# Optimization experiments

Measured on AMD Instinct MI355X. Metric: run time of the kernel, lower is better.

The kernel has to match this reference:

```python
import jax, jax.numpy as jnp
import numpy as np

B, L, D = 4, 2048, 512
NL, ED, N, R, K = 2, 1024, 16, 32, 4
EPS = 1e-5


def rmsnorm(x, w):
    return x * jax.lax.rsqrt(jnp.mean(x * x, axis=-1, keepdims=True) + EPS) * w


def mamba_block(u, in_w, conv_w, conv_b, xproj_w, dtproj_w, dtproj_b, A_log, Dp, out_w):
    # u: [B, L, D]
    xz = u @ in_w.T                              # [B, L, 2*ED]
    xp, z = jnp.split(xz, 2, axis=-1)
    # depthwise causal conv1d over time
    xc = jnp.transpose(xp, (0, 2, 1))            # [B, ED, L]
    w = conv_w[:, None, :]                       # [ED, 1, K]
    xc = jax.lax.conv_general_dilated(
        xc, w, window_strides=(1,), padding=[(K - 1, 0)],
        feature_group_count=ED, dimension_numbers=('NCH', 'OIH', 'NCH'))
    xc = jnp.transpose(xc, (0, 2, 1)) + conv_b   # [B, L, ED]
    xc = jax.nn.silu(xc)
    # input-dependent SSM params
    dbc = xc @ xproj_w.T                         # [B, L, R+2N]
    dt, Bm, Cm = jnp.split(dbc, [R, R + N], axis=-1)
    delta = jax.nn.softplus(dt @ dtproj_w.T + dtproj_b)  # [B, L, ED]
    A = -jnp.exp(A_log)                          # [ED, N]
    # sequential selective scan over time (carry h: [B, ED, N])
    dT = jnp.transpose(delta, (1, 0, 2))
    BT = jnp.transpose(Bm, (1, 0, 2))
    CT = jnp.transpose(Cm, (1, 0, 2))
    xT = jnp.transpose(xc, (1, 0, 2))

    def step(h, inp):
        d_t, B_t, C_t, x_t = inp                 # [B,ED], [B,N], [B,N], [B,ED]
        dA = jnp.exp(d_t[..., None] * A)         # [B, ED, N]
        h = dA * h + (d_t * x_t)[..., None] * B_t[:, None, :]
        y = jnp.einsum('ben,bn->be', h, C_t)
        return h, y

    h0 = jnp.zeros((u.shape[0], ED, N), u.dtype)
    _, yT = jax.lax.scan(step, h0, (dT, BT, CT, xT))
    y = jnp.transpose(yT, (1, 0, 2)) + Dp * xc   # [B, L, ED]
    y = y * jax.nn.silu(z)
    return y @ out_w.T                           # [B, L, D]


def setup_inputs() -> dict:
    key = jax.random.key(0)
    ks = jax.random.split(key, 10)
    s = 0.02
    return {
        'x': jax.random.normal(ks[0], (B, L, D), jnp.float32),
        'mask': jnp.ones((B, L), jnp.int32),
        'norm_w': jnp.ones((NL, D), jnp.float32),
        'in_w': jax.random.normal(ks[1], (NL, 2 * ED, D), jnp.float32) * s,
        'conv_w': jax.random.normal(ks[2], (NL, ED, K), jnp.float32) * 0.2,
        'conv_b': jnp.zeros((NL, ED), jnp.float32),
        'xproj_w': jax.random.normal(ks[3], (NL, R + 2 * N, ED), jnp.float32) * s,
        'dtproj_w': jax.random.normal(ks[4], (NL, ED, R), jnp.float32) * s,
        'dtproj_b': jax.random.normal(ks[5], (NL, ED), jnp.float32) * 0.1,
        'A_log': jnp.broadcast_to(jnp.log(jnp.arange(1, N + 1, dtype=jnp.float32)), (NL, ED, N)) + 0.0,
        'D_param': jnp.ones((NL, ED), jnp.float32),
        'out_w': jax.random.normal(ks[6], (NL, D, ED), jnp.float32) * s,
    }


def reference(x, mask, norm_w, in_w, conv_w, conv_b, xproj_w, dtproj_w,
              dtproj_b, A_log, D_param, out_w):
    m = mask.astype(x.dtype)[:, :, None]
    for i in range(norm_w.shape[0]):
        x = x * m
        # ResidualBlock: x + MambaBlock(RMSNorm(x)); dropout is identity at eval
        x = x + mamba_block(rmsnorm(x, norm_w[i]), in_w[i], conv_w[i], conv_b[i],
                            xproj_w[i], dtproj_w[i], dtproj_b[i], A_log[i],
                            D_param[i], out_w[i])
        x = x * m
    return x, x[:, 0, :]
```

## Files before the change

### kernel.cpp

```cpp
#include <hip/hip_runtime.h>
#include <math.h>

#define B_ 4
#define L_ 2048
#define D_ 512
#define ED_ 1024
#define N_ 16
#define R_ 32
#define KC_ 4
#define M_ (B_*L_)
#define NC_ 128
#define T_  (L_/NC_)
#define S_  (B_*ED_*N_)
#define BE_ (B_*ED_)
#define LOG2E 1.44269504f
#define LN2   0.69314718f

typedef __attribute__((ext_vector_type(8))) short short8;
typedef __attribute__((ext_vector_type(4))) float floatx4;
typedef __attribute__((ext_vector_type(2))) float floatv2;

static __device__ __forceinline__ float b2f(unsigned short u) {
    unsigned int v = ((unsigned int)u) << 16;
    float f;
    __builtin_memcpy(&f, &v, 4);
    return f;
}
static __device__ __forceinline__ unsigned short f2b(float f) {
    unsigned int u;
    __builtin_memcpy(&u, &f, 4);
    unsigned int lsb = (u >> 16) & 1u;
    u += 0x7fffu + lsb;
    return (unsigned short)(u >> 16);
}
static __device__ __forceinline__ float silu(float x) {
    return x / (1.f + exp2f(-LOG2E * x));
}
static __device__ __forceinline__ float softplusf(float x) {
    return fmaxf(x, 0.f) + LN2 * log2f(1.f + exp2f(-LOG2E * fabsf(x)));
}
static __device__ __forceinline__ void pow_tree2(float a1, floatv2* pw) {
    float a2 = a1 * a1, a4 = a2 * a2, a8 = a4 * a4;
    pw[0] = (floatv2){a1, a2};
    pw[1] = pw[0] * a2;
    pw[2] = pw[0] * a4;
    pw[3] = pw[1] * a4;
    pw[4] = pw[0] * a8;
    pw[5] = pw[1] * a8;
    pw[6] = pw[2] * a8;
    pw[7] = pw[3] * a8;
}

__global__ void k_flag0(int* flag) {
    if (blockIdx.x == 0 && threadIdx.x == 0) *flag = 0;
}
__global__ void k_detect(const unsigned short* __restrict__ x, int* flag) {
    int i = blockIdx.x * 256 + threadIdx.x;
    unsigned int e = (x[i] >> 7) & 0xFF;
    unsigned long long m = __ballot(e >= 0x88);
    if ((threadIdx.x & 63) == 0 && m != 0ull) atomicOr(flag, 1);
}

struct Seg9 { const void* src[9]; int prefix[10]; };
__global__ void k_cvt_batch(Seg9 segs, float* __restrict__ dst, int total,
                            const int* __restrict__ flag) {
    int i = blockIdx.x * 256 + threadIdx.x;
    if (i >= total) return;
    int s = 0;
#pragma unroll
    for (int k = 1; k < 9; ++k) if (i >= segs.prefix[k]) s = k;
    int off = i - segs.prefix[s];
    if (*flag) dst[i] = ((const float*)segs.src[s])[off];
    else       dst[i] = b2f(((const unsigned short*)segs.src[s])[off]);
}
__global__ void k_cvt_bf_batch(const void* __restrict__ src0,
                               const void* __restrict__ src1,
                               unsigned short* __restrict__ dst,
                               int n0, int total, const int* __restrict__ flag) {
    int i = blockIdx.x * 256 + threadIdx.x;
    if (i >= total) return;
    const void* src = (i < n0) ? src0 : src1;
    int off = (i < n0) ? i : i - n0;
    if (*flag) dst[i] = f2b(((const float*)src)[off]);
    else       dst[i] = ((const unsigned short*)src)[off];
}

__global__ void k_prep(const float* __restrict__ wdt,
                       const float* __restrict__ A_log,
                       float* __restrict__ wT,
                       float* __restrict__ A0s,
                       int* __restrict__ structf) {
    int idx = blockIdx.x * 256 + threadIdx.x;
    int layer = idx >> 10, e = idx & (ED_ - 1);
    const float* src = wdt + (size_t)idx * R_;
    float* dstb = wT + (size_t)layer * (R_ * ED_);
#pragma unroll
    for (int r = 0; r < R_; ++r)
        dstb[(r >> 2) * (ED_ * 4) + e * 4 + (r & 3)] = src[r];
    float A0 = -exp2f(LOG2E * A_log[(size_t)idx * N_]) * LOG2E;
    bool st = true;
#pragma unroll
    for (int n = 1; n < N_; ++n) {
        float An = -exp2f(LOG2E * A_log[(size_t)idx * N_ + n]) * LOG2E;
        st = st && (fabsf(An - (n + 1) * A0) <= 1e-4f * fabsf(An));
    }
    A0s[idx] = A0;
    structf[idx] = st ? 1 : 0;
}

__global__ __launch_bounds__(128) void k_rmsnorm(float* __restrict__ x,
                                                 const int* __restrict__ mask,
                                                 const float* __restrict__ w,
                                                 unsigned short* __restrict__ ubf) {
    int row = blockIdx.x;
    int tid = threadIdx.x;
    size_t base = (size_t)row * D_ + tid * 4;
    float4 v = *(const float4*)(x + base);
    float mv = (float)mask[row];
    v.x *= mv; v.y *= mv; v.z *= mv; v.w *= mv;
    *(float4*)(x + base) = v;
    float ss = v.x*v.x + v.y*v.y + v.z*v.z + v.w*v.w;
#pragma unroll
    for (int o = 1; o < 64; o <<= 1) ss += __shfl_xor(ss, o, 64);
    __shared__ float sred[2];
    if ((tid & 63) == 0) sred[tid >> 6] = ss;
    __syncthreads();
    float rs = rsqrtf((sred[0] + sred[1]) / (float)D_ + 1e-5f);
    float4 wv = *(const float4*)(w + tid * 4);
    ushort4 b4;
    b4.x = f2b(v.x * rs * wv.x);
    b4.y = f2b(v.y * rs * wv.y);
    b4.z = f2b(v.z * rs * wv.z);
    b4.w = f2b(v.w * rs * wv.w);
    *(ushort4*)(ubf + base) = b4;
}

typedef __attribute__((address_space(1))) const unsigned int guint;
typedef __attribute__((address_space(3))) unsigned int luint;
#define GLL(gp, lp) __builtin_amdgcn_global_load_lds((guint*)(const void*)(gp), (luint*)(void*)(lp), 16, 0, 0)

template<int N> static __device__ __forceinline__ void waitv() {
    if constexpr (N == 0) asm volatile("s_waitcnt vmcnt(0)" ::: "memory");
    else if constexpr (N == 3) asm volatile("s_waitcnt vmcnt(3)" ::: "memory");
    else if constexpr (N == 4) asm volatile("s_waitcnt vmcnt(4)" ::: "memory");
}

template<int MODE, int BNT>
__global__ __launch_bounds__(256) void gemm_bt(const unsigned short* __restrict__ A,
                                               const unsigned short* __restrict__ W,
                                               void* __restrict__ C,
                                               const int* __restrict__ mask,
                                               const int* __restrict__ flag,
                                               void* __restrict__ out,
                                               int M, int N, int K) {
    constexpr int NF = BNT / 32;
    constexpr int LW = 2 + BNT / 64;
    __shared__ unsigned short As[3][128][32];
    __shared__ unsigned short Bs[3][BNT][32];
    int tid  = threadIdx.x;
    int wave = tid >> 6;
    int lane = tid & 63;
    int nwg = gridDim.x * gridDim.y;
    int id  = blockIdx.y * gridDim.x + blockIdx.x;
    int swz = (id & 7) * (nwg >> 3) + (id >> 3);
    int m0 = (swz / gridDim.x) * 128;
    int n0 = (swz % gridDim.x) * BNT;
    int wm = (wave & 1) * 64;
    int wn = (wave >> 1) * (BNT / 2);
    int quad = lane >> 4;
    int l16  = lane & 15;
    int crd = (quad ^ ((l16 >> 1) & 3)) * 8;

    int rA0 = wave * 16 + (lane >> 2);
    int cA  = ((lane & 3) ^ ((rA0 >> 1) & 3)) * 8;

    floatx4 acc[4][NF] = {};

    auto stage = [&](int buf, int k0) {
        const unsigned short* gA0 = A + (size_t)(m0 + rA0) * K + k0 + cA;
        GLL(gA0,                   &As[buf][wave * 16][0]);
        GLL(gA0 + (size_t)64 * K,  &As[buf][64 + wave * 16][0]);
        const unsigned short* gB0 = W + (size_t)(n0 + rA0) * K + k0 + cA;
        GLL(gB0,                   &Bs[buf][wave * 16][0]);
        if constexpr (BNT == 128)
            GLL(gB0 + (size_t)64 * K, &Bs[buf][64 + wave * 16][0]);
    };

    int nk = K / 32;
    stage(0, 0);
    stage(1, 32);

    int cur = 0;
    for (int t = 0; t < nk; ++t) {
        if (t + 1 < nk) waitv<LW>();
        else            waitv<0>();
        asm volatile("s_barrier" ::: "memory");
        if (t + 2 < nk) {
            int bw = cur + 2; if (bw >= 3) bw -= 3;
            stage(bw, (t + 2) * 32);
        }
        short8 af[4], bfr[NF];
#pragma unroll
        for (int f = 0; f < 4; ++f)
            af[f]  = *(const short8*)&As[cur][wm + f * 16 + l16][crd];
#pragma unroll
        for (int f = 0; f < NF; ++f)
            bfr[f] = *(const short8*)&Bs[cur][wn + f * 16 + l16][crd];
#pragma unroll
        for (int mf = 0; mf < 4; ++mf)
#pragma unroll
            for (int nf = 0; nf < NF; ++nf)
                acc[mf][nf] = __builtin_amdgcn_mfma_f32_16x16x32_bf16(af[mf], bfr[nf], acc[mf][nf], 0, 0, 0);
        asm volatile("s_waitcnt lgkmcnt(0)" ::: "memory");
        cur = (cur == 2) ? 0 : cur + 1;
    }

    int fl = (MODE == 3) ? *flag : 0;
#pragma unroll
    for (int mf = 0; mf < 4; ++mf) {
#pragma unroll
        for (int nf = 0; nf < NF; ++nf) {
#pragma unroll
            for (int i = 0; i < 4; ++i) {
                int r = m0 + wm + mf * 16 + quad * 4 + i;
                int c = n0 + wn + nf * 16 + l16;
                size_t idx = (size_t)r * N + c;
                if (MODE == 1) {
                    ((unsigned short*)C)[idx] = f2b(acc[mf][nf][i]);
                } else if (MODE == 2) {
                    float* C32 = (float*)C;
                    float mv = (float)mask[r];
                    C32[idx] = (C32[idx] + acc[mf][nf][i]) * mv;
                } else {
                    const float* C32 = (const float*)C;
                    float mv = (float)mask[r];
                    float v = (C32[idx] + acc[mf][nf][i]) * mv;
                    if (fl) ((float*)out)[idx] = v;
                    else    ((unsigned short*)out)[idx] = f2b(v);
                    if ((r & (L_ - 1)) == 0) {
                        size_t oidx = (size_t)M_ * D_ + (size_t)(r >> 11) * D_ + c;
                        if (fl) ((float*)out)[oidx] = v;
                        else    ((unsigned short*)out)[oidx] = f2b(v);
                    }
                }
            }
        }
    }
}

#define BM 64
#define BN 64
#define BK 16
#define KS 8
__global__ __launch_bounds__(256) void gemm_nt_sk(const unsigned short* __restrict__ A,
                                                  const float* __restrict__ W,
                                                  float* __restrict__ part,
                                                  int M, int N, int K) {
    __shared__ float Asm[BK][BM + 4];
    __shared__ float Wsm[BK][BN + 4];
    int tid = threadIdx.x;
    int ks = blockIdx.x;
    int m0 = blockIdx.y * BM;
    int kb = ks * (K / KS);
    int ke = kb + (K / KS);
    int tx = tid & 15;
    int ty = tid >> 4;
    int lr = tid >> 2;
    int lk = (tid & 3) * 4;
    float acc[4][4] = {};
    for (int k0 = kb; k0 < ke; k0 += BK) {
        ushort4 av = *(const ushort4*)(A + (size_t)(m0 + lr) * K + k0 + lk);
        Asm[lk + 0][lr] = b2f(av.x); Asm[lk + 1][lr] = b2f(av.y);
        Asm[lk + 2][lr] = b2f(av.z); Asm[lk + 3][lr] = b2f(av.w);
        float4 wv = *(const float4*)(W + (size_t)lr * K + k0 + lk);
        Wsm[lk + 0][lr] = wv.x; Wsm[lk + 1][lr] = wv.y;
        Wsm[lk + 2][lr] = wv.z; Wsm[lk + 3][lr] = wv.w;
        __syncthreads();
#pragma unroll
        for (int kk = 0; kk < BK; ++kk) {
            float4 a = *(const float4*)&Asm[kk][ty * 4];
            float4 w = *(const float4*)&Wsm[kk][tx * 4];
            acc[0][0] += a.x * w.x; acc[0][1] += a.x * w.y; acc[0][2] += a.x * w.z; acc[0][3] += a.x * w.w;
            acc[1][0] += a.y * w.x; acc[1][1] += a.y * w.y; acc[1][2] += a.y * w.z; acc[1][3] += a.y * w.w;
            acc[2][0] += a.z * w.x; acc[2][1] += a.z * w.y; acc[2][2] += a.z * w.z; acc[2][3] += a.z * w.w;
            acc[3][0] += a.w * w.x; acc[3][1] += a.w * w.y; acc[3][2] += a.w * w.z; acc[3][3] += a.w * w.w;
        }
        __syncthreads();
    }
    float* p = part + (size_t)ks * M * N;
#pragma unroll
    for (int i = 0; i < 4; ++i) {
        int m = m0 + ty * 4 + i;
#pragma unroll
        for (int j = 0; j < 4; ++j) {
            int n = tx * 4 + j;
            p[(size_t)m * N + n] = acc[i][j];
        }
    }
}

__global__ void k_red8(const float* __restrict__ part, float* __restrict__ dbc, int mn4) {
    int i = blockIdx.x * 256 + threadIdx.x;
    if (i >= mn4) return;
    float4 s = ((const float4*)part)[i];
#pragma unroll
    for (int ks = 1; ks < KS; ++ks) {
        float4 v = ((const float4*)(part + (size_t)ks * mn4 * 4))[i];
        s.x += v.x; s.y += v.y; s.z += v.z; s.w += v.w;
    }
    ((float4*)dbc)[i] = s;
}

__global__ __launch_bounds__(256) void k_conv(const unsigned short* __restrict__ xzb,
                                              const float* __restrict__ cw,
                                              const float* __restrict__ cb,
                                              unsigned short* __restrict__ xcb) {
    int idx = blockIdx.x * 256 + threadIdx.x;
    int e2 = idx & (ED_ / 2 - 1);
    int e  = e2 * 2;
    int bl = idx >> 9;
    int l  = bl & (L_ - 1);
    float acc0 = cb[e], acc1 = cb[e + 1];
    const unsigned short* col = xzb + (size_t)bl * (2 * ED_) + e;
    float4 wa = *(const float4*)(cw + e * 4);
    float4 wb = *(const float4*)(cw + e * 4 + 4);
    ushort2 v3 = *(const ushort2*)(col);
    if (l >= 3) {
        ushort2 v0 = *(const ushort2*)(col - 3 * 2 * ED_);
        ushort2 v1 = *(const ushort2*)(col - 2 * 2 * ED_);
        ushort2 v2 = *(const ushort2*)(col - 1 * 2 * ED_);
        acc0 += wa.x * b2f(v0.x) + wa.y * b2f(v1.x) + wa.z * b2f(v2.x) + wa.w * b2f(v3.x);
        acc1 += wb.x * b2f(v0.y) + wb.y * b2f(v1.y) + wb.z * b2f(v2.y) + wb.w * b2f(v3.y);
    } else {
        if (l >= 2) {
            ushort2 v1 = *(const ushort2*)(col - 2 * 2 * ED_);
            acc0 += wa.y * b2f(v1.x); acc1 += wb.y * b2f(v1.y);
        }
        if (l >= 1) {
            ushort2 v2 = *(const ushort2*)(col - 1 * 2 * ED_);
            acc0 += wa.z * b2f(v2.x); acc1 += wb.z * b2f(v2.y);
        }
        acc0 += wa.w * b2f(v3.x); acc1 += wb.w * b2f(v3.y);
    }
    ushort2 o;
    o.x = f2b(silu(acc0));
    o.y = f2b(silu(acc1));
    *(ushort2*)(xcb + (size_t)bl * ED_ + e) = o;
}

__global__ __launch_bounds__(256) void k_scan_a(const unsigned short* __restrict__ xcb,
                                                const float* __restrict__ dbc,
                                                const float* __restrict__ wt,
                                                const float* __restrict__ dtb,
                                                const float* __restrict__ A0s,
                                                const int* __restrict__ structf,
                                                const float* __restrict__ A_log,
                                                float* __restrict__ sumdbuf,
                                                float* __restrict__ hl) {
    int b = blockIdx.z, c = blockIdx.y;
    int e = blockIdx.x * 256 + threadIdx.x;
    __shared__ float sRow[T_][64];
    size_t t0 = (size_t)b * L_ + (size_t)c * T_;
    {
        const float4* src = (const float4*)(dbc + t0 * 64);
        float4* dst = (float4*)&sRow[0][0];
#pragma unroll
        for (int i = 0; i < T_ * 16; i += 256)
            dst[i + threadIdx.x] = src[i + threadIdx.x];
    }
    __syncthreads();
    floatv2 w2[R_ / 2];
    {
        const float4* wtp = (const float4*)wt;
#pragma unroll
        for (int i = 0; i < 8; ++i) {
            float4 v = wtp[(size_t)i * ED_ + e];
            w2[2 * i]     = (floatv2){v.x, v.y};
            w2[2 * i + 1] = (floatv2){v.z, v.w};
        }
    }
    float bias = dtb[e];
    float A0 = A0s[e];
    bool structured = structf[e] != 0;
    floatv2 h2[8];
#pragma unroll
    for (int i = 0; i < 8; ++i) h2[i] = (floatv2){0.f, 0.f};
    float sumd = 0.f;
    if (structured) {
        const unsigned short* xp = xcb + t0 * ED_ + e;
        float xv_t = b2f(*xp); xp += ED_;
        for (int t = 0; t < T_; ++t) {
            unsigned short xr = (t + 1 < T_) ? *xp : (unsigned short)0; xp += ED_;
            const floatv2* dt2 = (const floatv2*)&sRow[t][0];
            floatv2 q0 = {0.f, 0.f}, q1 = {0.f, 0.f}, q2 = {0.f, 0.f}, q3 = {0.f, 0.f};
#pragma unroll
            for (int r = 0; r < R_ / 2; r += 4) {
                q0 += dt2[r + 0] * w2[r + 0];
                q1 += dt2[r + 1] * w2[r + 1];
                q2 += dt2[r + 2] * w2[r + 2];
                q3 += dt2[r + 3] * w2[r + 3];
            }
            floatv2 qs = (q0 + q1) + (q2 + q3);
            float d = softplusf(qs.x + qs.y + bias);
            float dx = d * xv_t;
            sumd += d;
            floatv2 pw[8];
            pow_tree2(exp2f(d * A0), pw);
            const floatv2* bb2 = (const floatv2*)&sRow[t][32];
#pragma unroll
            for (int i = 0; i < 8; ++i)
                h2[i] = pw[i] * h2[i] + dx * bb2[i];
            xv_t = b2f(xr);
        }
    } else {
        float A[N_];
        float* h = (float*)h2;
#pragma unroll
        for (int n = 0; n < N_; ++n) A[n] = -exp2f(LOG2E * A_log[e * N_ + n]) * LOG2E;
        float* wsc = (float*)w2;
        for (int t = 0; t < T_; ++t) {
            size_t bl = t0 + t;
            float p0 = bias, p1 = 0.f, p2 = 0.f, p3 = 0.f;
#pragma unroll
            for (int r = 0; r < R_; r += 4) {
                p0 += sRow[t][r + 0] * wsc[r + 0];
                p1 += sRow[t][r + 1] * wsc[r + 1];
                p2 += sRow[t][r + 2] * wsc[r + 2];
                p3 += sRow[t][r + 3] * wsc[r + 3];
            }
            float d = softplusf((p0 + p1) + (p2 + p3));
            float dx = d * b2f(xcb[bl * ED_ + e]);
            sumd += d;
#pragma unroll
            for (int n = 0; n < N_; ++n) {
                float a = exp2f(d * A[n]);
                h[n] = a * h[n] + dx * sRow[t][32 + n];
            }
        }
    }
    size_t base = (size_t)c * BE_ + (size_t)b * ED_ + e;
    const float* h = (const float*)h2;
#pragma unroll
    for (int n = 0; n < N_; ++n)
        hl[(size_t)n * (NC_ * BE_) + base] = h[n];
    sumdbuf[base] = sumd;
}

__global__ __launch_bounds__(256) void k_scan_b(const float* __restrict__ sumd,
                                                const float* __restrict__ hl,
                                                const float* __restrict__ A_log,
                                                float* __restrict__ carry) {
    int s = blockIdx.x * 256 + threadIdx.x;
    int n  = s >> 12;
    int be = s & (BE_ - 1);
    int e  = be & (ED_ - 1);
    float An = -exp2f(LOG2E * A_log[e * N_ + n]) * LOG2E;
    const float* hln = hl    + (size_t)n * (NC_ * BE_);
    float*       crn = carry + (size_t)n * (NC_ * BE_);
    float sdr[8], hlr[8];
#pragma unroll
    for (int c = 0; c < 8; ++c) {
        sdr[c] = sumd[(size_t)c * BE_ + be];
        hlr[c] = hln[(size_t)c * BE_ + be];
    }
    float h = 0.f;
#pragma unroll
    for (int c = 0; c < NC_; ++c) {
        int r = c & 7;
        crn[(size_t)c * BE_ + be] = h;
        float p = exp2f(sdr[r] * An), q = hlr[r];
        if (c + 8 < NC_) {
            sdr[r] = sumd[(size_t)(c + 8) * BE_ + be];
            hlr[r] = hln[(size_t)(c + 8) * BE_ + be];
        }
        h = p * h + q;
    }
}

__global__ __launch_bounds__(256) void k_scan_c(const unsigned short* __restrict__ xcb,
                                                const float* __restrict__ dbc,
                                                const unsigned short* __restrict__ xzb,
                                                const float* __restrict__ wt,
                                                const float* __restrict__ dtb,
                                                const float* __restrict__ A0s,
                                                const int* __restrict__ structf,
                                                const float* __restrict__ A_log,
                                                const float* __restrict__ Dp,
                                                const float* __restrict__ carry,
                                                unsigned short* __restrict__ ybf) {
    int b = blockIdx.z, c = blockIdx.y;
    int e = blockIdx.x * 256 + threadIdx.x;
    __shared__ float sRow[T_][64];
    size_t t0 = (size_t)b * L_ + (size_t)c * T_;
    {
        const float4* src = (const float4*)(dbc + t0 * 64);
        float4* dst = (float4*)&sRow[0][0];
#pragma unroll
        for (int i = 0; i < T_ * 16; i += 256)
            dst[i + threadIdx.x] = src[i + threadIdx.x];
    }
    __syncthreads();
    floatv2 w2[R_ / 2];
    {
        const float4* wtp = (const float4*)wt;
#pragma unroll
        for (int i = 0; i < 8; ++i) {
            float4 v = wtp[(size_t)i * ED_ + e];
            w2[2 * i]     = (floatv2){v.x, v.y};
            w2[2 * i + 1] = (floatv2){v.z, v.w};
        }
    }
    float bias = dtb[e];
    float A0 = A0s[e];
    bool structured = structf[e] != 0;
    floatv2 h2[8];
    size_t base = (size_t)c * BE_ + (size_t)b * ED_ + e;
    {
        float hs[N_];
#pragma unroll
        for (int n = 0; n < N_; ++n)
            hs[n] = carry[(size_t)n * (NC_ * BE_) + base];
#pragma unroll
        for (int i = 0; i < 8; ++i) h2[i] = (floatv2){hs[2 * i], hs[2 * i + 1]};
    }
    float Dv = Dp[e];
    if (structured) {
        const unsigned short* xp = xcb + t0 * ED_ + e;
        const unsigned short* zp = xzb + t0 * (2 * ED_) + ED_ + e;
        unsigned short* yp = ybf + t0 * ED_ + e;
        float xv_t = b2f(*xp); xp += ED_;
        unsigned short z_t = *zp; zp += 2 * ED_;
        for (int t = 0; t < T_; ++t) {
            unsigned short xr = 0, z_n = 0;
            if (t + 1 < T_) {
                xr  = *xp;
                z_n = *zp;
            }
            xp += ED_; zp += 2 * ED_;
            const floatv2* dt2 = (const floatv2*)&sRow[t][0];
            floatv2 q0 = {0.f, 0.f}, q1 = {0.f, 0.f}, q2 = {0.f, 0.f}, q3 = {0.f, 0.f};
#pragma unroll
            for (int r = 0; r < R_ / 2; r += 4) {
                q0 += dt2[r + 0] * w2[r + 0];
                q1 += dt2[r + 1] * w2[r + 1];
                q2 += dt2[r + 2] * w2[r + 2];
                q3 += dt2[r + 3] * w2[r + 3];
            }
            floatv2 qs = (q0 + q1) + (q2 + q3);
            float d_t = softplusf(qs.x + qs.y + bias);
            float dx = d_t * xv_t;
            floatv2 pw[8];
            pow_tree2(exp2f(d_t * A0), pw);
            const floatv2* bb2 = (const floatv2*)&sRow[t][32];
            const floatv2* cc2 = (const floatv2*)&sRow[t][48];
            floatv2 y0 = {0.f, 0.f}, y1 = {0.f, 0.f};
#pragma unroll
            for (int i = 0; i < 8; i += 2) {
                h2[i + 0] = pw[i + 0] * h2[i + 0] + dx * bb2[i + 0];
                h2[i + 1] = pw[i + 1] * h2[i + 1] + dx * bb2[i + 1];
                y0 += h2[i + 0] * cc2[i + 0];
                y1 += h2[i + 1] * cc2[i + 1];
            }
            floatv2 ys = y0 + y1;
            float y = ys.x + ys.y;
            float z = b2f(z_t);
            *yp = f2b((y + Dv * xv_t) * silu(z)); yp += ED_;
            xv_t = b2f(xr); z_t = z_n;
        }
    } else {
        float A[N_];
        float* h = (float*)h2;
#pragma unroll
        for (int n = 0; n < N_; ++n) A[n] = -exp2f(LOG2E * A_log[e * N_ + n]) * LOG2E;
        float* wsc = (float*)w2;
        for (int t = 0; t < T_; ++t) {
            size_t bl = t0 + t;
            float p0 = bias, p1 = 0.f, p2 = 0.f, p3 = 0.f;
#pragma unroll
            for (int r = 0; r < R_; r += 4) {
                p0 += sRow[t][r + 0] * wsc[r + 0];
                p1 += sRow[t][r + 1] * wsc[r + 1];
                p2 += sRow[t][r + 2] * wsc[r + 2];
                p3 += sRow[t][r + 3] * wsc[r + 3];
            }
            float d = softplusf((p0 + p1) + (p2 + p3));
            float xv = b2f(xcb[bl * ED_ + e]);
            float dx = d * xv;
            float y = 0.f;
#pragma unroll
            for (int n = 0; n < N_; ++n) {
                float a = exp2f(d * A[n]);
                h[n] = a * h[n] + dx * sRow[t][32 + n];
                y += h[n] * sRow[t][48 + n];
            }
            float z = b2f(xzb[bl * (2 * ED_) + ED_ + e]);
            ybf[bl * ED_ + e] = f2b((y + Dv * xv) * silu(z));
        }
    }
}

extern "C" void kernel_launch(void* const* d_in, const int* in_sizes, int n_in,
                              void* d_out, int out_size, void* d_ws, size_t ws_size,
                              hipStream_t stream) {
    const int* mask = (const int*)d_in[1];

    float* ws = (float*)d_ws;
    int*   flag = (int*)d_ws;
    float* xw   = ws + 16;
    float* wn   = xw   + (size_t)M_ * D_;
    float* wc   = wn   + 1024;
    float* wcb  = wc   + 8192;
    float* wx   = wcb  + 2048;
    float* wdt  = wx   + 131072;
    float* wdtb = wdt  + 65536;
    float* wal  = wdtb + 2048;
    float* wdp  = wal  + 32768;
    unsigned short* wib = (unsigned short*)(wdp + 2048);
    unsigned short* wob = wib + 2097152;
    unsigned short* ubf = wob + 1048576;
    unsigned short* xzb = ubf + (size_t)M_ * D_;
    unsigned short* xcb = xzb + (size_t)M_ * 2 * ED_;
    float* dbc  = (float*)(xcb + (size_t)M_ * ED_);
    float* hl   = dbc   + (size_t)M_ * 64;
    float* carry= hl    + (size_t)NC_ * S_;
    float* sumd = carry + (size_t)NC_ * S_;
    float* wT   = sumd  + (size_t)NC_ * BE_;
    float* A0s  = wT    + 2 * R_ * ED_;
    int*   stfl = (int*)(A0s + 2 * ED_);
    unsigned short* ybf = (unsigned short*)hl;
    float* part = carry;

    k_flag0<<<1, 1, 0, stream>>>(flag);
    k_detect<<<128, 256, 0, stream>>>((const unsigned short*)d_in[0], flag);

    {
        Seg9 segs;
        int idxs[9] = {0, 2, 4, 5, 6, 7, 8, 9, 10};
        int pre = 0;
        for (int i = 0; i < 9; ++i) {
            segs.src[i] = d_in[idxs[i]];
            segs.prefix[i] = pre;
            pre += in_sizes[idxs[i]];
        }
        segs.prefix[9] = pre;
        k_cvt_batch<<<(pre + 255) / 256, 256, 0, stream>>>(segs, xw, pre, flag);
        int n0 = 2 * 2 * ED_ * D_;
        int tot = n0 + 2 * D_ * ED_;
        k_cvt_bf_batch<<<(tot + 255) / 256, 256, 0, stream>>>(d_in[3], d_in[11], wib, n0, tot, flag);
    }
    k_prep<<<(2 * ED_) / 256, 256, 0, stream>>>(wdt, wal, wT, A0s, stfl);

    for (int layer = 0; layer < 2; ++layer) {
        const float* nw = wn  + layer * D_;
        const unsigned short* iw = wib + (size_t)layer * 2 * ED_ * D_;
        const float* cw = wc  + layer * ED_ * KC_;
        const float* cb = wcb + layer * ED_;
        const float* xwp= wx  + (size_t)layer * 64 * ED_;
        const float* db = wdtb+ layer * ED_;
        const float* al = wal + layer * ED_ * N_;
        const float* dp = wdp + layer * ED_;
        const float* wtl= wT  + (size_t)layer * R_ * ED_;
        const float* a0l= A0s + layer * ED_;
        const int*   sfl= stfl+ layer * ED_;
        const unsigned short* ow = wob + (size_t)layer * D_ * ED_;

        k_rmsnorm<<<M_, 128, 0, stream>>>(xw, mask, nw, ubf);
        gemm_bt<1, 128><<<dim3(2 * ED_ / 128, M_ / 128), 256, 0, stream>>>(ubf, iw, xzb, nullptr, nullptr, nullptr, M_, 2 * ED_, D_);
        k_conv<<<(M_ * ED_ / 2) / 256, 256, 0, stream>>>(xzb, cw, cb, xcb);
        gemm_nt_sk<<<dim3(KS, M_ / BM), 256, 0, stream>>>(xcb, xwp, part, M_, 64, ED_);
        k_red8<<<(M_ * 64 / 4 + 255) / 256, 256, 0, stream>>>(part, dbc, M_ * 64 / 4);
        k_scan_a<<<dim3(ED_ / 256, NC_, B_), 256, 0, stream>>>(xcb, dbc, wtl, db, a0l, sfl, al, sumd, hl);
        k_scan_b<<<S_ / 256, 256, 0, stream>>>(sumd, hl, al, carry);
        k_scan_c<<<dim3(ED_ / 256, NC_, B_), 256, 0, stream>>>(xcb, dbc, xzb, wtl, db, a0l, sfl, al, dp, carry, ybf);
        if (layer == 0) {
            gemm_bt<2, 64><<<dim3(D_ / 64, M_ / 128), 256, 0, stream>>>(ybf, ow, xw, mask, nullptr, nullptr, M_, D_, ED_);
        } else {
            gemm_bt<3, 64><<<dim3(D_ / 64, M_ / 128), 256, 0, stream>>>(ybf, ow, xw, mask, flag, d_out, M_, D_, ED_);
        }
    }
}
```

Before: 502.5 us.

## Store delta in first scan pass and reuse it in output scan

```diff
diff --git a/kernel.cpp b/kernel.cpp
--- a/kernel.cpp
+++ b/kernel.cpp
@@ -108,25 +108,26 @@
     structf[idx] = st ? 1 : 0;
 }
 
-__global__ __launch_bounds__(128) void k_rmsnorm(float* __restrict__ x,
+__global__ __launch_bounds__(256) void k_rmsnorm(const float* __restrict__ x,
                                                  const int* __restrict__ mask,
                                                  const float* __restrict__ w,
                                                  unsigned short* __restrict__ ubf) {
-    int row = blockIdx.x;
     int tid = threadIdx.x;
-    size_t base = (size_t)row * D_ + tid * 4;
+    int row = blockIdx.x * 2 + (tid >> 7);
+    int t128 = tid & 127;
+    size_t base = (size_t)row * D_ + t128 * 4;
     float4 v = *(const float4*)(x + base);
     float mv = (float)mask[row];
     v.x *= mv; v.y *= mv; v.z *= mv; v.w *= mv;
-    *(float4*)(x + base) = v;
     float ss = v.x*v.x + v.y*v.y + v.z*v.z + v.w*v.w;
 #pragma unroll
     for (int o = 1; o < 64; o <<= 1) ss += __shfl_xor(ss, o, 64);
-    __shared__ float sred[2];
+    __shared__ float sred[4];
     if ((tid & 63) == 0) sred[tid >> 6] = ss;
     __syncthreads();
-    float rs = rsqrtf((sred[0] + sred[1]) / (float)D_ + 1e-5f);
-    float4 wv = *(const float4*)(w + tid * 4);
+    int g = tid >> 7;
+    float rs = rsqrtf((sred[2 * g] + sred[2 * g + 1]) / (float)D_ + 1e-5f);
+    float4 wv = *(const float4*)(w + t128 * 4);
     ushort4 b4;
     b4.x = f2b(v.x * rs * wv.x);
     b4.y = f2b(v.y * rs * wv.y);
@@ -355,6 +356,7 @@
                                                 const float* __restrict__ A0s,
                                                 const int* __restrict__ structf,
                                                 const float* __restrict__ A_log,
+                                                float* __restrict__ delta,
                                                 float* __restrict__ sumdbuf,
                                                 float* __restrict__ hl) {
     int b = blockIdx.z, c = blockIdx.y;
@@ -388,6 +390,7 @@
     float sumd = 0.f;
     if (structured) {
         const unsigned short* xp = xcb + t0 * ED_ + e;
+        float* dep = delta + t0 * ED_ + e;
         float xv_t = b2f(*xp); xp += ED_;
         for (int t = 0; t < T_; ++t) {
             unsigned short xr = (t + 1 < T_) ? *xp : (unsigned short)0; xp += ED_;
@@ -402,6 +405,7 @@
             }
             floatv2 qs = (q0 + q1) + (q2 + q3);
             float d = softplusf(qs.x + qs.y + bias);
+            *dep = d; dep += ED_;
             float dx = d * xv_t;
             sumd += d;
             floatv2 pw[8];
@@ -429,6 +433,7 @@
                 p3 += sRow[t][r + 3] * wsc[r + 3];
             }
             float d = softplusf((p0 + p1) + (p2 + p3));
+            delta[bl * ED_ + e] = d;
             float dx = d * b2f(xcb[bl * ED_ + e]);
             sumd += d;
 #pragma unroll
@@ -478,10 +483,9 @@
 }
 
 __global__ __launch_bounds__(256) void k_scan_c(const unsigned short* __restrict__ xcb,
+                                                const float* __restrict__ delta,
                                                 const float* __restrict__ dbc,
                                                 const unsigned short* __restrict__ xzb,
-                                                const float* __restrict__ wt,
-                                                const float* __restrict__ dtb,
                                                 const float* __restrict__ A0s,
                                                 const int* __restrict__ structf,
                                                 const float* __restrict__ A_log,
@@ -490,27 +494,16 @@
                                                 unsigned short* __restrict__ ybf) {
     int b = blockIdx.z, c = blockIdx.y;
     int e = blockIdx.x * 256 + threadIdx.x;
-    __shared__ float sRow[T_][64];
+    __shared__ float sBC[T_][32];
     size_t t0 = (size_t)b * L_ + (size_t)c * T_;
     {
-        const float4* src = (const float4*)(dbc + t0 * 64);
-        float4* dst = (float4*)&sRow[0][0];
-#pragma unroll
-        for (int i = 0; i < T_ * 16; i += 256)
-            dst[i + threadIdx.x] = src[i + threadIdx.x];
+        int i = threadIdx.x;
+        if (i < T_ * 8) {
+            int t = i >> 3, q = i & 7;
+            ((float4*)&sBC[t][0])[q] = *(const float4*)(dbc + (t0 + t) * 64 + 32 + q * 4);
+        }
     }
     __syncthreads();
-    floatv2 w2[R_ / 2];
-    {
-        const float4* wtp = (const float4*)wt;
-#pragma unroll
-        for (int i = 0; i < 8; ++i) {
-            float4 v = wtp[(size_t)i * ED_ + e];
-            w2[2 * i]     = (floatv2){v.x, v.y};
-            w2[2 * i + 1] = (floatv2){v.z, v.w};
-        }
-    }
-    float bias = dtb[e];
     float A0 = A0s[e];
     bool structured = structf[e] != 0;
     floatv2 h2[8];
@@ -526,33 +519,26 @@
     float Dv = Dp[e];
     if (structured) {
         const unsigned short* xp = xcb + t0 * ED_ + e;
+        const float* dp_ = delta + t0 * ED_ + e;
         const unsigned short* zp = xzb + t0 * (2 * ED_) + ED_ + e;
         unsigned short* yp = ybf + t0 * ED_ + e;
         float xv_t = b2f(*xp); xp += ED_;
+        float d_t  = *dp_;     dp_ += ED_;
         unsigned short z_t = *zp; zp += 2 * ED_;
         for (int t = 0; t < T_; ++t) {
             unsigned short xr = 0, z_n = 0;
+            float d_n = 0.f;
             if (t + 1 < T_) {
                 xr  = *xp;
+                d_n = *dp_;
                 z_n = *zp;
             }
-            xp += ED_; zp += 2 * ED_;
-            const floatv2* dt2 = (const floatv2*)&sRow[t][0];
-            floatv2 q0 = {0.f, 0.f}, q1 = {0.f, 0.f}, q2 = {0.f, 0.f}, q3 = {0.f, 0.f};
-#pragma unroll
-            for (int r = 0; r < R_ / 2; r += 4) {
-                q0 += dt2[r + 0] * w2[r + 0];
-                q1 += dt2[r + 1] * w2[r + 1];
-                q2 += dt2[r + 2] * w2[r + 2];
-                q3 += dt2[r + 3] * w2[r + 3];
-            }
-            floatv2 qs = (q0 + q1) + (q2 + q3);
-            float d_t = softplusf(qs.x + qs.y + bias);
+            xp += ED_; dp_ += ED_; zp += 2 * ED_;
             float dx = d_t * xv_t;
             floatv2 pw[8];
             pow_tree2(exp2f(d_t * A0), pw);
-            const floatv2* bb2 = (const floatv2*)&sRow[t][32];
-            const floatv2* cc2 = (const floatv2*)&sRow[t][48];
+            const floatv2* bb2 = (const floatv2*)&sBC[t][0];
+            const floatv2* cc2 = (const floatv2*)&sBC[t][16];
             floatv2 y0 = {0.f, 0.f}, y1 = {0.f, 0.f};
 #pragma unroll
             for (int i = 0; i < 8; i += 2) {
@@ -565,33 +551,24 @@
             float y = ys.x + ys.y;
             float z = b2f(z_t);
             *yp = f2b((y + Dv * xv_t) * silu(z)); yp += ED_;
-            xv_t = b2f(xr); z_t = z_n;
+            xv_t = b2f(xr); d_t = d_n; z_t = z_n;
         }
     } else {
         float A[N_];
         float* h = (float*)h2;
 #pragma unroll
         for (int n = 0; n < N_; ++n) A[n] = -exp2f(LOG2E * A_log[e * N_ + n]) * LOG2E;
-        float* wsc = (float*)w2;
         for (int t = 0; t < T_; ++t) {
             size_t bl = t0 + t;
-            float p0 = bias, p1 = 0.f, p2 = 0.f, p3 = 0.f;
-#pragma unroll
-            for (int r = 0; r < R_; r += 4) {
-                p0 += sRow[t][r + 0] * wsc[r + 0];
-                p1 += sRow[t][r + 1] * wsc[r + 1];
-                p2 += sRow[t][r + 2] * wsc[r + 2];
-                p3 += sRow[t][r + 3] * wsc[r + 3];
-            }
-            float d = softplusf((p0 + p1) + (p2 + p3));
+            float d  = delta[bl * ED_ + e];
             float xv = b2f(xcb[bl * ED_ + e]);
             float dx = d * xv;
             float y = 0.f;
 #pragma unroll
             for (int n = 0; n < N_; ++n) {
                 float a = exp2f(d * A[n]);
-                h[n] = a * h[n] + dx * sRow[t][32 + n];
-                y += h[n] * sRow[t][48 + n];
+                h[n] = a * h[n] + dx * sBC[t][n];
+                y += h[n] * sBC[t][16 + n];
             }
             float z = b2f(xzb[bl * (2 * ED_) + ED_ + e]);
             ybf[bl * ED_ + e] = f2b((y + Dv * xv) * silu(z));
@@ -627,6 +604,7 @@
     float* wT   = sumd  + (size_t)NC_ * BE_;
     float* A0s  = wT    + 2 * R_ * ED_;
     int*   stfl = (int*)(A0s + 2 * ED_);
+    float* delta= (float*)(stfl + 2 * ED_);
     unsigned short* ybf = (unsigned short*)hl;
     float* part = carry;
 
@@ -664,14 +642,14 @@
         const int*   sfl= stfl+ layer * ED_;
         const unsigned short* ow = wob + (size_t)layer * D_ * ED_;
 
-        k_rmsnorm<<<M_, 128, 0, stream>>>(xw, mask, nw, ubf);
+        k_rmsnorm<<<M_ / 2, 256, 0, stream>>>(xw, mask, nw, ubf);
         gemm_bt<1, 128><<<dim3(2 * ED_ / 128, M_ / 128), 256, 0, stream>>>(ubf, iw, xzb, nullptr, nullptr, nullptr, M_, 2 * ED_, D_);
         k_conv<<<(M_ * ED_ / 2) / 256, 256, 0, stream>>>(xzb, cw, cb, xcb);
         gemm_nt_sk<<<dim3(KS, M_ / BM), 256, 0, stream>>>(xcb, xwp, part, M_, 64, ED_);
         k_red8<<<(M_ * 64 / 4 + 255) / 256, 256, 0, stream>>>(part, dbc, M_ * 64 / 4);
-        k_scan_a<<<dim3(ED_ / 256, NC_, B_), 256, 0, stream>>>(xcb, dbc, wtl, db, a0l, sfl, al, sumd, hl);
+        k_scan_a<<<dim3(ED_ / 256, NC_, B_), 256, 0, stream>>>(xcb, dbc, wtl, db, a0l, sfl, al, delta, sumd, hl);
         k_scan_b<<<S_ / 256, 256, 0, stream>>>(sumd, hl, al, carry);
-        k_scan_c<<<dim3(ED_ / 256, NC_, B_), 256, 0, stream>>>(xcb, dbc, xzb, wtl, db, a0l, sfl, al, dp, carry, ybf);
+        k_scan_c<<<dim3(ED_ / 256, NC_, B_), 256, 0, stream>>>(xcb, delta, dbc, xzb, a0l, sfl, al, dp, carry, ybf);
         if (layer == 0) {
             gemm_bt<2, 64><<<dim3(D_ / 64, M_ / 128), 256, 0, stream>>>(ybf, ow, xw, mask, nullptr, nullptr, M_, D_, ED_);
         } else {
```

New measurement: 485.7 us. 1.03x faster.
